# Performance work log

Hardware: AMD Instinct MI355X
Metric: run time of the kernel (lower is better)

Reference implementation:

```python
import jax, jax.numpy as jnp
import numpy as np

N_LAYERS = 4
D_MODEL = 256
P = 128            # ssm_size // 2 (conj_sym S5)
LATENT_DIM = 256
MAX_SEQ_LEN = 32768
OUTPUT_DIM = 64
LN_EPS = 1e-6      # flax nn.LayerNorm default


def layer_norm(x, scale, bias):
    mu = jnp.mean(x, axis=-1, keepdims=True)
    var = jnp.mean(jnp.square(x - mu), axis=-1, keepdims=True)
    return (x - mu) * jax.lax.rsqrt(var + LN_EPS) * scale + bias


def s5_ssm(u, Lre, Lim, Bre, Bim, Cre, Cim, Dvec, log_step, resets):
    """u: (L, H) float. Returns (L, H) float. conj_sym S5, zoh discretization."""
    step = jnp.exp(log_step)                       # (P,)
    Lam = Lre + 1j * Lim                           # (P,) complex
    Lam_bar = jnp.exp(Lam * step)                  # (P,)
    B_bar = ((Lam_bar - 1.0) / Lam)[:, None] * (Bre + 1j * Bim)  # (P, H)
    Bu = u @ B_bar.T                               # (L, P) complex
    A = jnp.broadcast_to(Lam_bar, Bu.shape)        # (L, P)
    c = resets[:, None].astype(u.dtype)            # (L, 1)

    def binop(qi, qj):
        Ai, bi, ci = qi
        Aj, bj, cj = qj
        return (Aj * Ai * (1.0 - cj) + Aj * cj,
                (Aj * bi + bj) * (1.0 - cj) + bj * cj,
                ci * (1.0 - cj) + cj)

    # zero initial hidden state => no prepend needed (identical result)
    _, xs, _ = jax.lax.associative_scan(binop, (A, Bu, c))
    y = 2.0 * jnp.real(xs @ (Cre + 1j * Cim).T)    # (L, H), conj_sym doubling
    return y + u * Dvec


def setup_inputs() -> dict:
    key = jax.random.key(0)
    ks = jax.random.split(key, 16)
    f = jax.random.normal
    return {
        "latent": f(ks[0], (LATENT_DIM,), jnp.float32),
        "W_expand": f(ks[1], (LATENT_DIM, D_MODEL), jnp.float32) / np.sqrt(LATENT_DIM),
        "b_expand": jnp.zeros((D_MODEL,), jnp.float32),
        "norm_scale": jnp.ones((N_LAYERS, D_MODEL), jnp.float32),
        "norm_bias": jnp.zeros((N_LAYERS, D_MODEL), jnp.float32),
        "Lambda_re": -(0.1 + 0.9 * jax.random.uniform(ks[2], (N_LAYERS, P))),
        "Lambda_im": np.pi * f(ks[3], (N_LAYERS, P), jnp.float32),
        "B_re": f(ks[4], (N_LAYERS, P, D_MODEL), jnp.float32) / np.sqrt(D_MODEL),
        "B_im": f(ks[5], (N_LAYERS, P, D_MODEL), jnp.float32) / np.sqrt(D_MODEL),
        "C_re": f(ks[6], (N_LAYERS, D_MODEL, P), jnp.float32) / np.sqrt(P),
        "C_im": f(ks[7], (N_LAYERS, D_MODEL, P), jnp.float32) / np.sqrt(P),
        "D": f(ks[8], (N_LAYERS, D_MODEL), jnp.float32),
        "log_step": jnp.log(jax.random.uniform(ks[9], (N_LAYERS, P), minval=1e-3, maxval=1e-1)),
        "W1": f(ks[10], (N_LAYERS, D_MODEL, D_MODEL), jnp.float32) / np.sqrt(D_MODEL),
        "b1": jnp.zeros((N_LAYERS, D_MODEL), jnp.float32),
        "W2": f(ks[11], (N_LAYERS, D_MODEL, D_MODEL), jnp.float32) / np.sqrt(D_MODEL),
        "b2": jnp.zeros((N_LAYERS, D_MODEL), jnp.float32),
        "W_out": f(ks[12], (D_MODEL, OUTPUT_DIM), jnp.float32) / np.sqrt(D_MODEL),
        "b_out": jnp.zeros((OUTPUT_DIM,), jnp.float32),
        "seq_len": MAX_SEQ_LEN,
    }


def reference(latent, W_expand, b_expand, norm_scale, norm_bias,
              Lambda_re, Lambda_im, B_re, B_im, C_re, C_im, D, log_step,
              W1, b1, W2, b2, W_out, b_out, seq_len):
    # latent_expand + leaky_relu, then broadcast to full trajectory
    x = jax.nn.leaky_relu(latent @ W_expand + b_expand)        # (H,)
    x = jnp.broadcast_to(x[None, :], (MAX_SEQ_LEN, D_MODEL))    # (L, H); batch dim of 1 dropped
    resets = jnp.zeros((MAX_SEQ_LEN,), x.dtype)                 # dones = zeros
    for i in range(N_LAYERS):
        skip = x
        h = layer_norm(x, norm_scale[i], norm_bias[i])          # prenorm
        y = s5_ssm(h, Lambda_re[i], Lambda_im[i], B_re[i], B_im[i],
                   C_re[i], C_im[i], D[i], log_step[i], resets)
        y = layer_norm(y, norm_scale[i], norm_bias[i])          # gtrxl norm (shared params)
        y = jax.nn.gelu(y)
        y = (y @ W1[i] + b1[i]) * jax.nn.sigmoid(y @ W2[i] + b2[i])  # full_glu
        x = skip + y
    return x @ W_out + b_out                                    # (L, output_dim)
```

## Files before the change

kernel.cpp:

```cpp
#include <hip/hip_runtime.h>
#include <stdint.h>

#define LSEQ 32768
#define NCH 512
#define TCH 64

typedef _Float16 half8 __attribute__((ext_vector_type(8)));
typedef _Float16 half4v __attribute__((ext_vector_type(4)));
typedef _Float16 half2v __attribute__((ext_vector_type(2)));
typedef float f32x4 __attribute__((ext_vector_type(4)));
typedef float f32x2 __attribute__((ext_vector_type(2)));

__device__ __forceinline__ float sigmoidf_(float x) { return 1.f / (1.f + __expf(-x)); }
__device__ __forceinline__ float gelu_(float x) {
    float z = 0.7978845608028654f * (x + 0.044715f * x * x * x);
    float e = __expf(2.f * z);
    float t = 1.f - 2.f / (e + 1.f);
    return 0.5f * x * (1.f + t);
}

__device__ __forceinline__ void gll16(const _Float16* gp, _Float16* lp) {
    __builtin_amdgcn_global_load_lds((__attribute__((address_space(1))) void*)gp,
                                     (__attribute__((address_space(3))) void*)lp, 16, 0, 0);
}

__global__ __launch_bounds__(512) void s5_k0a(const float* __restrict__ lre, const float* __restrict__ lim,
                                              const float* __restrict__ lstep,
                                              float* aR, float* aI, float* cbR, float* cbI,
                                              float* aTR, float* aTI, float* alp, float* ralp) {
    int i = threadIdx.x;
    float st = expf(lstep[i]);
    float lr = lre[i] * st, li = lim[i] * st;
    float ea = expf(lr);
    float ar = ea * cosf(li), ai = ea * sinf(li);
    float den = lre[i] * lre[i] + lim[i] * lim[i];
    float nr = ar - 1.f, ni = ai;
    float cr = (nr * lre[i] + ni * lim[i]) / den;
    float ci = (ni * lre[i] - nr * lim[i]) / den;
    float cm = sqrtf(cr * cr + ci * ci);
    float al = sqrtf(2.83f / fmaxf(cm, 1e-8f));
    float eT = expf(lr * (float)TCH);
    aR[i] = ar; aI[i] = ai;
    cbR[i] = cr; cbI[i] = ci;
    aTR[i] = eT * cosf(li * (float)TCH);
    aTI[i] = eT * sinf(li * (float)TCH);
    alp[i] = al; ralp[i] = 1.f / al;
}

__global__ __launch_bounds__(256) void s5_k0b(const float* __restrict__ Bre, const float* __restrict__ Bim,
                                              const float* __restrict__ Cre, const float* __restrict__ Cim,
                                              const float* __restrict__ W1, const float* __restrict__ W2,
                                              const float* __restrict__ b1, const float* __restrict__ b2,
                                              const float* __restrict__ Wout,
                                              const float* __restrict__ cbR, const float* __restrict__ cbI,
                                              const float* __restrict__ alp, const float* __restrict__ ralp,
                                              _Float16* Wbu, _Float16* Wc, _Float16* Wglu,
                                              _Float16* WoutT, float* bglu) {
    int stride = gridDim.x * blockDim.x;
    int tid0 = blockIdx.x * blockDim.x + threadIdx.x;
    for (int i = tid0; i < 262144; i += stride) {
        int l = i >> 16, n = (i >> 8) & 255, k = i & 255;
        int s = n >> 4, lmn = n & 15;
        int p = l * 128 + (s >> 1) * 16 + lmn;
        float re = cbR[p] * Bre[p * 256 + k] - cbI[p] * Bim[p * 256 + k];
        float im = cbR[p] * Bim[p * 256 + k] + cbI[p] * Bre[p * 256 + k];
        Wbu[i] = (_Float16)(((s & 1) ? im : re) * alp[p]);
    }
    for (int i = tid0; i < 262144; i += stride) {
        int l = i >> 16, n = (i >> 8) & 255, k = i & 255;
        int p = k >> 1;
        float base = (k & 1) ? -2.f * Cim[(l * 256 + n) * 128 + p]
                             : 2.f * Cre[(l * 256 + n) * 128 + p];
        Wc[i] = (_Float16)(base * ralp[l * 128 + p]);
    }
    for (int i = tid0; i < 524288; i += stride) {
        int l = i >> 17, n = (i >> 8) & 511, k = i & 255;
        int j = ((n >> 7) << 6) | (((n >> 6) & 1) << 5) | (((n >> 5) & 1) << 4) | (n & 15);
        const float* src = ((n >> 4) & 1) ? W2 : W1;
        Wglu[i] = (_Float16)src[(l * 256 + k) * 256 + j];
    }
    for (int i = tid0; i < 16384; i += stride) {
        int n = i >> 8, k = i & 255;
        WoutT[i] = (_Float16)Wout[k * 64 + n];
    }
    for (int i = tid0; i < 2048; i += stride) {
        int l = i >> 9, n = i & 511;
        int j = ((n >> 7) << 6) | (((n >> 6) & 1) << 5) | (((n >> 5) & 1) << 4) | (n & 15);
        bglu[i] = (((n >> 4) & 1) ? b2 : b1)[l * 256 + j];
    }
}

__global__ __launch_bounds__(256) void s5_k0c(const float* __restrict__ latent, const float* __restrict__ W,
                                              const float* __restrict__ b, _Float16* __restrict__ x0h) {
    __shared__ float lat[256];
    lat[threadIdx.x] = latent[threadIdx.x];
    __syncthreads();
    float s = b[threadIdx.x];
    for (int k = 0; k < 256; ++k) s += lat[k] * W[k * 256 + threadIdx.x];
    x0h[threadIdx.x] = (_Float16)((s > 0.f) ? s : 0.01f * s);
}

__global__ __launch_bounds__(256) void s5_k1_fill(const _Float16* __restrict__ x0h, _Float16* __restrict__ x) {
    int i = blockIdx.x * 256 + threadIdx.x;
    half8 v = *(const half8*)(x0h + (i & 31) * 8);
    *(half8*)(x + i * 8) = v;
}

__global__ __launch_bounds__(512, 2) void s5_k3_lngemm(const _Float16* __restrict__ x,
                                                       const _Float16* __restrict__ Wt,
                                                       const float* __restrict__ gamma,
                                                       const float* __restrict__ beta,
                                                       _Float16* __restrict__ h,
                                                       _Float16* __restrict__ Buh) {
    __shared__ _Float16 sW[64 * 512];
    int tid = threadIdx.x, wid = tid >> 6, lane = tid & 63;
    int lm = lane & 15, quad = lane >> 4;
    int m0 = blockIdx.x * 128;
    int rowb = m0 + wid * 16;

    auto stageW = [&](int half) {
#pragma unroll
        for (int i = 0; i < 8; ++i) {
            int c = i * 8 + wid;
            int ks = c >> 3, n16 = c & 7;
            gll16(Wt + (half * 128 + n16 * 16 + lm) * 256 + ks * 32 + quad * 8, sW + c * 512);
        }
    };
    stageW(0);

    int row = rowb + lm;
    half8 af[8];
    {
        half8 xv[8];
#pragma unroll
        for (int ks = 0; ks < 8; ++ks)
            xv[ks] = *(const half8*)(x + row * 256 + ks * 32 + quad * 8);
        float s1 = 0.f, s2 = 0.f;
#pragma unroll
        for (int i = 0; i < 8; ++i)
#pragma unroll
            for (int j = 0; j < 8; ++j) { float t = (float)xv[i][j]; s1 += t; s2 += t * t; }
        s1 += __shfl_xor(s1, 16, 64); s2 += __shfl_xor(s2, 16, 64);
        s1 += __shfl_xor(s1, 32, 64); s2 += __shfl_xor(s2, 32, 64);
        float mu = s1 * (1.f / 256.f);
        float var = s2 * (1.f / 256.f) - mu * mu;
        float rs = rsqrtf(fmaxf(var, 0.f) + 1e-6f);
#pragma unroll
        for (int ks = 0; ks < 8; ++ks) {
            f32x4 g0 = *(const f32x4*)(gamma + ks * 32 + quad * 8);
            f32x4 g1 = *(const f32x4*)(gamma + ks * 32 + quad * 8 + 4);
            f32x4 b0 = *(const f32x4*)(beta + ks * 32 + quad * 8);
            f32x4 b1 = *(const f32x4*)(beta + ks * 32 + quad * 8 + 4);
            half8 o;
#pragma unroll
            for (int j = 0; j < 4; ++j) {
                o[j]     = (_Float16)(((float)xv[ks][j] - mu) * rs * g0[j] + b0[j]);
                o[j + 4] = (_Float16)(((float)xv[ks][j + 4] - mu) * rs * g1[j] + b1[j]);
            }
            af[ks] = o;
            *(half8*)(h + row * 256 + ks * 32 + quad * 8) = o;
        }
    }
    asm volatile("s_waitcnt vmcnt(0)" ::: "memory");
    __syncthreads();

    f32x4 zero = {0.f, 0.f, 0.f, 0.f};
    f32x4 acc[2][8];
#pragma unroll
    for (int hf = 0; hf < 2; ++hf)
#pragma unroll
        for (int nt = 0; nt < 8; ++nt) acc[hf][nt] = zero;

#pragma unroll
    for (int ks = 0; ks < 8; ++ks) {
        half8 bf[8];
#pragma unroll
        for (int nt = 0; nt < 8; ++nt)
            bf[nt] = *(const half8*)(sW + (ks * 8 + nt) * 512 + lane * 8);
#pragma unroll
        for (int nt = 0; nt < 8; ++nt)
            acc[0][nt] = __builtin_amdgcn_mfma_f32_16x16x32_f16(af[ks], bf[nt], acc[0][nt], 0, 0, 0);
    }
    __syncthreads();
    stageW(1);
    asm volatile("s_waitcnt vmcnt(0)" ::: "memory");
    __syncthreads();
#pragma unroll
    for (int ks = 0; ks < 8; ++ks) {
        half8 bf[8];
#pragma unroll
        for (int nt = 0; nt < 8; ++nt)
            bf[nt] = *(const half8*)(sW + (ks * 8 + nt) * 512 + lane * 8);
#pragma unroll
        for (int nt = 0; nt < 8; ++nt)
            acc[1][nt] = __builtin_amdgcn_mfma_f32_16x16x32_f16(af[ks], bf[nt], acc[1][nt], 0, 0, 0);
    }

#pragma unroll
    for (int u = 0; u < 8; ++u) {
        int hf = u >> 2, q = u & 3;
        int p = u * 16 + lm;
#pragma unroll
        for (int r = 0; r < 4; ++r) {
            half2v o = {(_Float16)acc[hf][2 * q][r], (_Float16)acc[hf][2 * q + 1][r]};
            *(half2v*)(Buh + (rowb + quad * 4 + r) * 256 + 2 * p) = o;
        }
    }
}

__global__ __launch_bounds__(128, 4) void s5_k4_carry(const _Float16* __restrict__ Bu,
                                                      const float* __restrict__ aR, const float* __restrict__ aI,
                                                      float* __restrict__ carRI) {
    int p = threadIdx.x, c = blockIdx.x;
    int t0 = c * TCH;
    const _Float16* bp = Bu + t0 * 256 + 2 * p;
    half2v hv[TCH];
#pragma unroll
    for (int j = 0; j < TCH; ++j) hv[j] = *(const half2v*)(bp + j * 256);
    float ar = aR[p], ai = aI[p];
    float sr = 0.f, si = 0.f;
#pragma unroll
    for (int j = 0; j < TCH; ++j) {
        float nr = fmaf(ar, sr, fmaf(-ai, si, (float)hv[j][0]));
        float ni = fmaf(ar, si, fmaf(ai, sr, (float)hv[j][1]));
        sr = nr; si = ni;
    }
    *(f32x2*)(carRI + (c * 128 + p) * 2) = f32x2{sr, si};
}

__global__ __launch_bounds__(128, 4) void s5_k6_scan(const _Float16* __restrict__ Bu,
                                                     const float* __restrict__ carRI,
                                                     const float* __restrict__ aR, const float* __restrict__ aI,
                                                     const float* __restrict__ aTR, const float* __restrict__ aTI,
                                                     _Float16* __restrict__ xs2) {
    int p = threadIdx.x, c = blockIdx.x;
    int t0 = c * TCH;
    const _Float16* bp = Bu + t0 * 256 + 2 * p;
    half2v hv[TCH];
#pragma unroll
    for (int j = 0; j < TCH; ++j) hv[j] = *(const half2v*)(bp + j * 256);
    float tr = aTR[p], ti = aTI[p];
    float cr = 0.f, ci = 0.f;
#pragma unroll 8
    for (int i = 0; i < c; ++i) {
        f32x2 w = *(const f32x2*)(carRI + (i * 128 + p) * 2);
        float nr = fmaf(tr, cr, fmaf(-ti, ci, w[0]));
        float ni = fmaf(tr, ci, fmaf(ti, cr, w[1]));
        cr = nr; ci = ni;
    }
    float ar = aR[p], ai = aI[p];
    float sr = cr, si = ci;
    _Float16* op = xs2 + t0 * 256 + 2 * p;
#pragma unroll
    for (int j = 0; j < TCH; ++j) {
        float nr = fmaf(ar, sr, fmaf(-ai, si, (float)hv[j][0]));
        float ni = fmaf(ar, si, fmaf(ai, sr, (float)hv[j][1]));
        sr = nr; si = ni;
        *(half2v*)(op + j * 256) = half2v{(_Float16)sr, (_Float16)si};
    }
}

__global__ __launch_bounds__(512, 2) void s5_k7_gemm_c(const _Float16* __restrict__ A,
                                                       const _Float16* __restrict__ Wt,
                                                       const _Float16* __restrict__ h,
                                                       const float* __restrict__ Dv,
                                                       const float* __restrict__ gamma,
                                                       const float* __restrict__ beta,
                                                       _Float16* __restrict__ g) {
    __shared__ _Float16 sW[64 * 512];
    int tid = threadIdx.x, wid = tid >> 6, lane = tid & 63;
    int lm = lane & 15, quad = lane >> 4;
    int m0 = blockIdx.x * 128;
    int rowb = m0 + wid * 16;

    auto stageW = [&](int half) {
#pragma unroll
        for (int i = 0; i < 8; ++i) {
            int c = i * 8 + wid;
            int ks = c >> 3, n16 = c & 7;
            gll16(Wt + (half * 128 + n16 * 16 + lm) * 256 + ks * 32 + quad * 8, sW + c * 512);
        }
    };
    stageW(0);
    half8 af[8];
#pragma unroll
    for (int ks = 0; ks < 8; ++ks)
        af[ks] = *(const half8*)(A + (rowb + lm) * 256 + ks * 32 + quad * 8);
    asm volatile("s_waitcnt vmcnt(0)" ::: "memory");
    __syncthreads();

    f32x4 zero = {0.f, 0.f, 0.f, 0.f};
    f32x4 acc[2][8];
#pragma unroll
    for (int hf = 0; hf < 2; ++hf)
#pragma unroll
        for (int nt = 0; nt < 8; ++nt) acc[hf][nt] = zero;

#pragma unroll
    for (int ks = 0; ks < 8; ++ks) {
        half8 bf[8];
#pragma unroll
        for (int nt = 0; nt < 8; ++nt)
            bf[nt] = *(const half8*)(sW + (ks * 8 + nt) * 512 + lane * 8);
#pragma unroll
        for (int nt = 0; nt < 8; ++nt)
            acc[0][nt] = __builtin_amdgcn_mfma_f32_16x16x32_f16(af[ks], bf[nt], acc[0][nt], 0, 0, 0);
    }
    __syncthreads();
    stageW(1);
    asm volatile("s_waitcnt vmcnt(0)" ::: "memory");
    __syncthreads();
#pragma unroll
    for (int ks = 0; ks < 8; ++ks) {
        half8 bf[8];
#pragma unroll
        for (int nt = 0; nt < 8; ++nt)
            bf[nt] = *(const half8*)(sW + (ks * 8 + nt) * 512 + lane * 8);
#pragma unroll
        for (int nt = 0; nt < 8; ++nt)
            acc[1][nt] = __builtin_amdgcn_mfma_f32_16x16x32_f16(af[ks], bf[nt], acc[1][nt], 0, 0, 0);
    }

#pragma unroll
    for (int hf = 0; hf < 2; ++hf)
#pragma unroll
        for (int nt = 0; nt < 8; ++nt) {
            int col = hf * 128 + nt * 16 + lm;
            float dv = Dv[col];
#pragma unroll
            for (int r = 0; r < 4; ++r)
                acc[hf][nt][r] += (float)h[(rowb + quad * 4 + r) * 256 + col] * dv;
        }
    float mu[4], rs[4];
#pragma unroll
    for (int r = 0; r < 4; ++r) {
        float a = 0.f, b = 0.f;
#pragma unroll
        for (int hf = 0; hf < 2; ++hf)
#pragma unroll
            for (int nt = 0; nt < 8; ++nt) {
                float v = acc[hf][nt][r];
                a += v; b += v * v;
            }
#pragma unroll
        for (int off = 1; off < 16; off <<= 1) {
            a += __shfl_xor(a, off, 64);
            b += __shfl_xor(b, off, 64);
        }
        float m = a * (1.f / 256.f);
        float var = b * (1.f / 256.f) - m * m;
        mu[r] = m;
        rs[r] = rsqrtf(fmaxf(var, 0.f) + 1e-6f);
    }
#pragma unroll
    for (int hf = 0; hf < 2; ++hf)
#pragma unroll
        for (int nt = 0; nt < 8; ++nt) {
            int col = hf * 128 + nt * 16 + lm;
            float ga = gamma[col], be = beta[col];
#pragma unroll
            for (int r = 0; r < 4; ++r) {
                float hn = (acc[hf][nt][r] - mu[r]) * rs[r] * ga + be;
                g[(rowb + quad * 4 + r) * 256 + col] = (_Float16)gelu_(hn);
            }
        }
}

__global__ __launch_bounds__(256, 2) void s5_k8_gemm_glu(const _Float16* __restrict__ A,
                                                         const _Float16* __restrict__ Wt,
                                                         const float* __restrict__ bias,
                                                         _Float16* __restrict__ x) {
    __shared__ _Float16 sW[64 * 512];
    int tid = threadIdx.x, wid = tid >> 6, lane = tid & 63;
    int lm = lane & 15, quad = lane >> 4;
    int n0 = blockIdx.y * 128;
    int m0 = blockIdx.x * 128;
#pragma unroll
    for (int i = 0; i < 16; ++i) {
        int c = i * 4 + wid;
        int ks = c >> 3, n16 = c & 7;
        gll16(Wt + (n0 + n16 * 16 + lm) * 256 + ks * 32 + quad * 8, sW + c * 512);
    }
    int rowb = m0 + wid * 32;
    half8 af[2][8];
#pragma unroll
    for (int mt = 0; mt < 2; ++mt)
#pragma unroll
        for (int ks = 0; ks < 8; ++ks)
            af[mt][ks] = *(const half8*)(A + (rowb + mt * 16 + lm) * 256 + ks * 32 + quad * 8);
    asm volatile("s_waitcnt vmcnt(0)" ::: "memory");
    __syncthreads();

    f32x4 zero = {0.f, 0.f, 0.f, 0.f};
    f32x4 acc[2][8];
#pragma unroll
    for (int mt = 0; mt < 2; ++mt)
#pragma unroll
        for (int nt = 0; nt < 8; ++nt) acc[mt][nt] = zero;
#pragma unroll
    for (int ks = 0; ks < 8; ++ks) {
        half8 bf[8];
#pragma unroll
        for (int nt = 0; nt < 8; ++nt)
            bf[nt] = *(const half8*)(sW + (ks * 8 + nt) * 512 + lane * 8);
#pragma unroll
        for (int mt = 0; mt < 2; ++mt)
#pragma unroll
            for (int nt = 0; nt < 8; ++nt)
                acc[mt][nt] = __builtin_amdgcn_mfma_f32_16x16x32_f16(af[mt][ks], bf[nt], acc[mt][nt], 0, 0, 0);
    }
    int jbase = (n0 >> 1) + lm;
    _Float16 xold[2][4][4];
#pragma unroll
    for (int mt = 0; mt < 2; ++mt)
#pragma unroll
        for (int q = 0; q < 4; ++q)
#pragma unroll
            for (int r = 0; r < 4; ++r)
                xold[mt][q][r] = x[(rowb + mt * 16 + quad * 4 + r) * 256 + jbase + q * 16];
#pragma unroll
    for (int mt = 0; mt < 2; ++mt)
#pragma unroll
        for (int q = 0; q < 4; ++q) {
            float b1v = bias[n0 + (2 * q) * 16 + lm];
            float b2v = bias[n0 + (2 * q + 1) * 16 + lm];
            int jcol = jbase + q * 16;
#pragma unroll
            for (int r = 0; r < 4; ++r) {
                float u1 = acc[mt][2 * q][r] + b1v;
                float u2 = acc[mt][2 * q + 1][r] + b2v;
                float gl = u1 * sigmoidf_(u2);
                int idx = (rowb + mt * 16 + quad * 4 + r) * 256 + jcol;
                x[idx] = (_Float16)((float)xold[mt][q][r] + gl);
            }
        }
}

__global__ __launch_bounds__(256, 2) void s5_k9_gemm_out(const _Float16* __restrict__ A,
                                                         const _Float16* __restrict__ Wt,
                                                         const float* __restrict__ bout,
                                                         float* __restrict__ out) {
    __shared__ _Float16 sW[32 * 512];
    int tid = threadIdx.x, wid = tid >> 6, lane = tid & 63;
    int lm = lane & 15, quad = lane >> 4;
    int m0 = blockIdx.x * 128;
#pragma unroll
    for (int i = 0; i < 8; ++i) {
        int c = i * 4 + wid;
        int ks = c >> 2, n16 = c & 3;
        gll16(Wt + (n16 * 16 + lm) * 256 + ks * 32 + quad * 8, sW + c * 512);
    }
    int rowb = m0 + wid * 32;
    half8 af[2][8];
#pragma unroll
    for (int mt = 0; mt < 2; ++mt)
#pragma unroll
        for (int ks = 0; ks < 8; ++ks)
            af[mt][ks] = *(const half8*)(A + (rowb + mt * 16 + lm) * 256 + ks * 32 + quad * 8);
    asm volatile("s_waitcnt vmcnt(0)" ::: "memory");
    __syncthreads();

    f32x4 zero = {0.f, 0.f, 0.f, 0.f};
    f32x4 acc[2][4];
#pragma unroll
    for (int mt = 0; mt < 2; ++mt)
#pragma unroll
        for (int nt = 0; nt < 4; ++nt) acc[mt][nt] = zero;
#pragma unroll
    for (int ks = 0; ks < 8; ++ks) {
        half8 bf[4];
#pragma unroll
        for (int nt = 0; nt < 4; ++nt)
            bf[nt] = *(const half8*)(sW + (ks * 4 + nt) * 512 + lane * 8);
#pragma unroll
        for (int mt = 0; mt < 2; ++mt)
#pragma unroll
            for (int nt = 0; nt < 4; ++nt)
                acc[mt][nt] = __builtin_amdgcn_mfma_f32_16x16x32_f16(af[mt][ks], bf[nt], acc[mt][nt], 0, 0, 0);
    }
#pragma unroll
    for (int mt = 0; mt < 2; ++mt)
#pragma unroll
        for (int nt = 0; nt < 4; ++nt) {
            int col = nt * 16 + lm;
            float bv = bout[col];
#pragma unroll
            for (int r = 0; r < 4; ++r) {
                int row = rowb + mt * 16 + quad * 4 + r;
                out[row * 64 + col] = acc[mt][nt][r] + bv;
            }
        }
}

constexpr size_t OFF_X    = 0;
constexpr size_t OFF_BU   = 33554432;
constexpr size_t OFF_H    = 67108864;
constexpr size_t OFF_WBU  = 100663296;
constexpr size_t OFF_WC   = OFF_WBU + 524288;
constexpr size_t OFF_WGLU = OFF_WC + 524288;
constexpr size_t OFF_WOUT = OFF_WGLU + 1048576;
constexpr size_t OFF_BGLU = OFF_WOUT + 32768;
constexpr size_t OFF_AR   = OFF_BGLU + 8192;
constexpr size_t OFF_AI   = OFF_AR + 2048;
constexpr size_t OFF_CBR  = OFF_AI + 2048;
constexpr size_t OFF_CBI  = OFF_CBR + 2048;
constexpr size_t OFF_ATR  = OFF_CBI + 2048;
constexpr size_t OFF_ATI  = OFF_ATR + 2048;
constexpr size_t OFF_ALP  = OFF_ATI + 2048;
constexpr size_t OFF_RALP = OFF_ALP + 2048;
constexpr size_t OFF_X0H  = OFF_RALP + 2048;
constexpr size_t OFF_CARRI= OFF_X0H + 1024;

extern "C" void kernel_launch(void* const* d_in, const int* in_sizes, int n_in,
                              void* d_out, int out_size, void* d_ws, size_t ws_size,
                              hipStream_t stream) {
    (void)in_sizes; (void)n_in; (void)out_size; (void)ws_size;
    const float* latent    = (const float*)d_in[0];
    const float* W_expand  = (const float*)d_in[1];
    const float* b_expand  = (const float*)d_in[2];
    const float* norm_s    = (const float*)d_in[3];
    const float* norm_b    = (const float*)d_in[4];
    const float* Lre       = (const float*)d_in[5];
    const float* Lim       = (const float*)d_in[6];
    const float* Bre       = (const float*)d_in[7];
    const float* Bim       = (const float*)d_in[8];
    const float* Cre       = (const float*)d_in[9];
    const float* Cim       = (const float*)d_in[10];
    const float* Dv        = (const float*)d_in[11];
    const float* lstep     = (const float*)d_in[12];
    const float* W1        = (const float*)d_in[13];
    const float* b1        = (const float*)d_in[14];
    const float* W2        = (const float*)d_in[15];
    const float* b2        = (const float*)d_in[16];
    const float* Wout      = (const float*)d_in[17];
    const float* bout      = (const float*)d_in[18];

    char* ws = (char*)d_ws;
    _Float16* x    = (_Float16*)(ws + OFF_X);
    _Float16* Buh  = (_Float16*)(ws + OFF_BU);
    _Float16* xs2  = (_Float16*)(ws + OFF_BU);
    _Float16* gbuf = (_Float16*)(ws + OFF_BU + 16777216);
    _Float16* hbuf = (_Float16*)(ws + OFF_H);
    _Float16* Wbu  = (_Float16*)(ws + OFF_WBU);
    _Float16* Wc   = (_Float16*)(ws + OFF_WC);
    _Float16* Wglu = (_Float16*)(ws + OFF_WGLU);
    _Float16* WoutT= (_Float16*)(ws + OFF_WOUT);
    float* bglu = (float*)(ws + OFF_BGLU);
    float* aR  = (float*)(ws + OFF_AR);
    float* aI  = (float*)(ws + OFF_AI);
    float* cbR = (float*)(ws + OFF_CBR);
    float* cbI = (float*)(ws + OFF_CBI);
    float* aTR = (float*)(ws + OFF_ATR);
    float* aTI = (float*)(ws + OFF_ATI);
    float* alp = (float*)(ws + OFF_ALP);
    float* ralp= (float*)(ws + OFF_RALP);
    _Float16* x0h = (_Float16*)(ws + OFF_X0H);
    float* carRI=(float*)(ws + OFF_CARRI);

    s5_k0a<<<1, 512, 0, stream>>>(Lre, Lim, lstep, aR, aI, cbR, cbI, aTR, aTI, alp, ralp);
    s5_k0b<<<256, 256, 0, stream>>>(Bre, Bim, Cre, Cim, W1, W2, b1, b2, Wout,
                                    cbR, cbI, alp, ralp, Wbu, Wc, Wglu, WoutT, bglu);
    s5_k0c<<<1, 256, 0, stream>>>(latent, W_expand, b_expand, x0h);
    s5_k1_fill<<<4096, 256, 0, stream>>>(x0h, x);

    for (int l = 0; l < 4; ++l) {
        s5_k3_lngemm<<<256, 512, 0, stream>>>(x, Wbu + l * 65536,
                                              norm_s + l * 256, norm_b + l * 256,
                                              hbuf, Buh);
        s5_k4_carry<<<NCH, 128, 0, stream>>>(Buh, aR + l * 128, aI + l * 128, carRI);
        s5_k6_scan<<<NCH, 128, 0, stream>>>(Buh, carRI, aR + l * 128, aI + l * 128,
                                            aTR + l * 128, aTI + l * 128, xs2);
        s5_k7_gemm_c<<<256, 512, 0, stream>>>(xs2, Wc + l * 65536, hbuf, Dv + l * 256,
                                              norm_s + l * 256, norm_b + l * 256, gbuf);
        s5_k8_gemm_glu<<<dim3(256, 4), 256, 0, stream>>>(gbuf, Wglu + l * 131072,
                                                         bglu + l * 512, x);
    }
    s5_k9_gemm_out<<<256, 256, 0, stream>>>(x, WoutT, bout, (float*)d_out);
}
```

Baseline: 512.0 us.

## Fuse chunk scan into C-projection GEMM and stage full Bu weights at once

The chunked scan (carry propagation plus intra-chunk recurrence) now runs inside the C-projection GEMM kernel. Its results go into a swizzled LDS tile that feeds the MFMA A operand directly, which removes the xs2 global round trip and one launch per layer. The LN+Bu GEMM kernel now stages both weight halves into LDS up front instead of reloading mid-kernel. Both kernels now use 64KB+ of shared memory at one block per CU. Only 256 of 512 threads do the serial scan while the rest wait, so occupancy and latency hiding drop.

```diff
diff --git a/kernel.cpp b/kernel.cpp
--- a/kernel.cpp
+++ b/kernel.cpp
@@ -106,27 +106,27 @@
     *(half8*)(x + i * 8) = v;
 }
 
-__global__ __launch_bounds__(512, 2) void s5_k3_lngemm(const _Float16* __restrict__ x,
+__global__ __launch_bounds__(512, 1) void s5_k3_lngemm(const _Float16* __restrict__ x,
                                                        const _Float16* __restrict__ Wt,
                                                        const float* __restrict__ gamma,
                                                        const float* __restrict__ beta,
                                                        _Float16* __restrict__ h,
                                                        _Float16* __restrict__ Buh) {
-    __shared__ _Float16 sW[64 * 512];
+    __shared__ _Float16 sW[128 * 512];
     int tid = threadIdx.x, wid = tid >> 6, lane = tid & 63;
     int lm = lane & 15, quad = lane >> 4;
     int m0 = blockIdx.x * 128;
     int rowb = m0 + wid * 16;
 
-    auto stageW = [&](int half) {
+#pragma unroll
+    for (int half = 0; half < 2; ++half)
 #pragma unroll
         for (int i = 0; i < 8; ++i) {
             int c = i * 8 + wid;
             int ks = c >> 3, n16 = c & 7;
-            gll16(Wt + (half * 128 + n16 * 16 + lm) * 256 + ks * 32 + quad * 8, sW + c * 512);
-        }
-    };
-    stageW(0);
+            gll16(Wt + (half * 128 + n16 * 16 + lm) * 256 + ks * 32 + quad * 8,
+                  sW + half * 32768 + c * 512);
+        }
 
     int row = rowb + lm;
     half8 af[8];
@@ -172,29 +172,17 @@
         for (int nt = 0; nt < 8; ++nt) acc[hf][nt] = zero;
 
 #pragma unroll
-    for (int ks = 0; ks < 8; ++ks) {
-        half8 bf[8];
-#pragma unroll
-        for (int nt = 0; nt < 8; ++nt)
-            bf[nt] = *(const half8*)(sW + (ks * 8 + nt) * 512 + lane * 8);
-#pragma unroll
-        for (int nt = 0; nt < 8; ++nt)
-            acc[0][nt] = __builtin_amdgcn_mfma_f32_16x16x32_f16(af[ks], bf[nt], acc[0][nt], 0, 0, 0);
-    }
-    __syncthreads();
-    stageW(1);
-    asm volatile("s_waitcnt vmcnt(0)" ::: "memory");
-    __syncthreads();
-#pragma unroll
-    for (int ks = 0; ks < 8; ++ks) {
-        half8 bf[8];
-#pragma unroll
-        for (int nt = 0; nt < 8; ++nt)
-            bf[nt] = *(const half8*)(sW + (ks * 8 + nt) * 512 + lane * 8);
-#pragma unroll
-        for (int nt = 0; nt < 8; ++nt)
-            acc[1][nt] = __builtin_amdgcn_mfma_f32_16x16x32_f16(af[ks], bf[nt], acc[1][nt], 0, 0, 0);
-    }
+    for (int hf = 0; hf < 2; ++hf)
+#pragma unroll
+        for (int ks = 0; ks < 8; ++ks) {
+            half8 bf[8];
+#pragma unroll
+            for (int nt = 0; nt < 8; ++nt)
+                bf[nt] = *(const half8*)(sW + hf * 32768 + (ks * 8 + nt) * 512 + lane * 8);
+#pragma unroll
+            for (int nt = 0; nt < 8; ++nt)
+                acc[hf][nt] = __builtin_amdgcn_mfma_f32_16x16x32_f16(af[ks], bf[nt], acc[hf][nt], 0, 0, 0);
+        }
 
 #pragma unroll
     for (int u = 0; u < 8; ++u) {
@@ -228,46 +216,18 @@
     *(f32x2*)(carRI + (c * 128 + p) * 2) = f32x2{sr, si};
 }
 
-__global__ __launch_bounds__(128, 4) void s5_k6_scan(const _Float16* __restrict__ Bu,
-                                                     const float* __restrict__ carRI,
-                                                     const float* __restrict__ aR, const float* __restrict__ aI,
-                                                     const float* __restrict__ aTR, const float* __restrict__ aTI,
-                                                     _Float16* __restrict__ xs2) {
-    int p = threadIdx.x, c = blockIdx.x;
-    int t0 = c * TCH;
-    const _Float16* bp = Bu + t0 * 256 + 2 * p;
-    half2v hv[TCH];
-#pragma unroll
-    for (int j = 0; j < TCH; ++j) hv[j] = *(const half2v*)(bp + j * 256);
-    float tr = aTR[p], ti = aTI[p];
-    float cr = 0.f, ci = 0.f;
-#pragma unroll 8
-    for (int i = 0; i < c; ++i) {
-        f32x2 w = *(const f32x2*)(carRI + (i * 128 + p) * 2);
-        float nr = fmaf(tr, cr, fmaf(-ti, ci, w[0]));
-        float ni = fmaf(tr, ci, fmaf(ti, cr, w[1]));
-        cr = nr; ci = ni;
-    }
-    float ar = aR[p], ai = aI[p];
-    float sr = cr, si = ci;
-    _Float16* op = xs2 + t0 * 256 + 2 * p;
-#pragma unroll
-    for (int j = 0; j < TCH; ++j) {
-        float nr = fmaf(ar, sr, fmaf(-ai, si, (float)hv[j][0]));
-        float ni = fmaf(ar, si, fmaf(ai, sr, (float)hv[j][1]));
-        sr = nr; si = ni;
-        *(half2v*)(op + j * 256) = half2v{(_Float16)sr, (_Float16)si};
-    }
-}
-
-__global__ __launch_bounds__(512, 2) void s5_k7_gemm_c(const _Float16* __restrict__ A,
+__global__ __launch_bounds__(512, 1) void s5_k7_gemm_c(const _Float16* __restrict__ Bu,
+                                                       const float* __restrict__ carRI,
                                                        const _Float16* __restrict__ Wt,
                                                        const _Float16* __restrict__ h,
+                                                       const float* __restrict__ aR, const float* __restrict__ aI,
+                                                       const float* __restrict__ aTR, const float* __restrict__ aTI,
                                                        const float* __restrict__ Dv,
                                                        const float* __restrict__ gamma,
                                                        const float* __restrict__ beta,
                                                        _Float16* __restrict__ g) {
     __shared__ _Float16 sW[64 * 512];
+    __shared__ _Float16 xsT[128 * 256];
     int tid = threadIdx.x, wid = tid >> 6, lane = tid & 63;
     int lm = lane & 15, quad = lane >> 4;
     int m0 = blockIdx.x * 128;
@@ -282,12 +242,45 @@
         }
     };
     stageW(0);
+
+    if (tid < 256) {
+        int cc = tid >> 7, p = tid & 127;
+        int cg = blockIdx.x * 2 + cc;
+        const _Float16* bp = Bu + (m0 + cc * TCH) * 256 + 2 * p;
+        half2v hv[TCH];
+#pragma unroll
+        for (int j = 0; j < TCH; ++j) hv[j] = *(const half2v*)(bp + j * 256);
+        float tr = aTR[p], ti = aTI[p];
+        float cr = 0.f, ci = 0.f;
+#pragma unroll 8
+        for (int i = 0; i < cg; ++i) {
+            f32x2 w = *(const f32x2*)(carRI + (i * 128 + p) * 2);
+            float nr = fmaf(tr, cr, fmaf(-ti, ci, w[0]));
+            float ni = fmaf(tr, ci, fmaf(ti, cr, w[1]));
+            cr = nr; ci = ni;
+        }
+        float ar = aR[p], ai = aI[p];
+        float sr = cr, si = ci;
+#pragma unroll
+        for (int j = 0; j < TCH; ++j) {
+            float nr = fmaf(ar, sr, fmaf(-ai, si, (float)hv[j][0]));
+            float ni = fmaf(ar, si, fmaf(ai, sr, (float)hv[j][1]));
+            sr = nr; si = ni;
+            int rl = cc * TCH + j;
+            int byte = (4 * p) ^ ((rl & 7) << 4);
+            *(half2v*)((char*)xsT + rl * 512 + byte) = half2v{(_Float16)sr, (_Float16)si};
+        }
+    }
+    asm volatile("s_waitcnt vmcnt(0)" ::: "memory");
+    __syncthreads();
+
+    int rl = wid * 16 + lm;
     half8 af[8];
 #pragma unroll
-    for (int ks = 0; ks < 8; ++ks)
-        af[ks] = *(const half8*)(A + (rowb + lm) * 256 + ks * 32 + quad * 8);
-    asm volatile("s_waitcnt vmcnt(0)" ::: "memory");
-    __syncthreads();
+    for (int ks = 0; ks < 8; ++ks) {
+        int b = ks * 64 + quad * 16;
+        af[ks] = *(const half8*)((const char*)xsT + rl * 512 + (b ^ ((rl & 7) << 4)));
+    }
 
     f32x4 zero = {0.f, 0.f, 0.f, 0.f};
     f32x4 acc[2][8];
@@ -538,7 +531,6 @@
     char* ws = (char*)d_ws;
     _Float16* x    = (_Float16*)(ws + OFF_X);
     _Float16* Buh  = (_Float16*)(ws + OFF_BU);
-    _Float16* xs2  = (_Float16*)(ws + OFF_BU);
     _Float16* gbuf = (_Float16*)(ws + OFF_BU + 16777216);
     _Float16* hbuf = (_Float16*)(ws + OFF_H);
     _Float16* Wbu  = (_Float16*)(ws + OFF_WBU);
@@ -568,9 +560,10 @@
                                               norm_s + l * 256, norm_b + l * 256,
                                               hbuf, Buh);
         s5_k4_carry<<<NCH, 128, 0, stream>>>(Buh, aR + l * 128, aI + l * 128, carRI);
-        s5_k6_scan<<<NCH, 128, 0, stream>>>(Buh, carRI, aR + l * 128, aI + l * 128,
-                                            aTR + l * 128, aTI + l * 128, xs2);
-        s5_k7_gemm_c<<<256, 512, 0, stream>>>(xs2, Wc + l * 65536, hbuf, Dv + l * 256,
+        s5_k7_gemm_c<<<256, 512, 0, stream>>>(Buh, carRI, Wc + l * 65536, hbuf,
+                                              aR + l * 128, aI + l * 128,
+                                              aTR + l * 128, aTI + l * 128,
+                                              Dv + l * 256,
                                               norm_s + l * 256, norm_b + l * 256, gbuf);
         s5_k8_gemm_glu<<<dim3(256, 4), 256, 0, stream>>>(gbuf, Wglu + l * 131072,
                                                          bglu + l * 512, x);
```

Result: faster. 477.3 us (-6.8%).
